# Optimization experiments

Measured on AMD Instinct MI355X. Metric: run time of the kernel, lower is better.

## Reference

```python
import jax, jax.numpy as jnp
import numpy as np
import math

N_HEAD = 16
N_CTX = 1024


def setup_inputs() -> dict:
    key = jax.random.key(0)
    ks = jax.random.split(key, 3)
    B, S, NX = 4, 1024, 1024
    x = jax.random.normal(ks[0], (B, S, NX), dtype=jnp.float32)
    # Conv1D weights stored as [nx, nf], init std=0.02, bias zeros
    c_attn_w = jax.random.normal(ks[1], (NX, 3 * NX), dtype=jnp.float32) * 0.02
    c_attn_b = jnp.zeros((3 * NX,), dtype=jnp.float32)
    c_proj_w = jax.random.normal(ks[2], (NX, NX), dtype=jnp.float32) * 0.02
    c_proj_b = jnp.zeros((NX,), dtype=jnp.float32)
    return {"x": x, "c_attn_w": c_attn_w, "c_attn_b": c_attn_b,
            "c_proj_w": c_proj_w, "c_proj_b": c_proj_b}


def reference(x, c_attn_w, c_attn_b, c_proj_w, c_proj_b):
    B, S, NX = x.shape
    H = N_HEAD
    D = NX // H
    # c_attn: Conv1D -> x @ W + b, then split into q, k, v
    qkv = x @ c_attn_w + c_attn_b                      # [B,S,3*NX]
    q, k, v = jnp.split(qkv, 3, axis=-1)               # each [B,S,NX]
    # split heads: q,v -> [B,H,S,D]; k -> [B,H,D,S]
    q = q.reshape(B, S, H, D).transpose(0, 2, 1, 3)
    k = k.reshape(B, S, H, D).transpose(0, 2, 3, 1)
    v = v.reshape(B, S, H, D).transpose(0, 2, 1, 3)
    # _attn: scores, scale, combined multiplicative+additive causal mask, softmax
    w = jnp.matmul(q, k)                               # [B,H,S,S]
    w = w / math.sqrt(D)                               # scale=True
    bias = jnp.tril(jnp.ones((S, S), dtype=w.dtype))[None, None]  # causal tril slice
    w = w * bias - 1e10 * (1.0 - bias)
    w = jax.nn.softmax(w, axis=-1)
    a = jnp.matmul(w, v)                               # [B,H,S,D]
    # merge heads
    a = a.transpose(0, 2, 1, 3).reshape(B, S, NX)
    # c_proj
    return a @ c_proj_w + c_proj_b
```

## Files before the change

kernel.cpp:

```cpp
#include <hip/hip_runtime.h>
#include <cstdint>

typedef __attribute__((ext_vector_type(8))) short short8;
typedef __attribute__((ext_vector_type(4))) short short4x;
typedef __attribute__((ext_vector_type(4))) float floatx4;

__device__ __forceinline__ unsigned short f2b(float f) {
    unsigned int u = __builtin_bit_cast(unsigned int, f);
    u += 0x7fffu + ((u >> 16) & 1u);
    return (unsigned short)(u >> 16);
}
__device__ __forceinline__ float b2f(unsigned short s) {
    unsigned int u = ((unsigned int)s) << 16;
    return __builtin_bit_cast(float, u);
}
__device__ __forceinline__ float fast_exp2(float x) {
    float r;
    asm("v_exp_f32 %0, %1" : "=v"(r) : "v"(x));
    return r;
}
__device__ __forceinline__ unsigned int pack_bf16_trunc(float lo, float hi) {
    return __builtin_amdgcn_perm(__builtin_bit_cast(unsigned int, hi),
                                 __builtin_bit_cast(unsigned int, lo), 0x07060302u);
}

#define GLDS(g, l) __builtin_amdgcn_global_load_lds(                                   \
    (const __attribute__((address_space(1))) unsigned int*)(g),                        \
    (__attribute__((address_space(3))) unsigned int*)(l), 16, 0, 0)

__global__ __launch_bounds__(256) void prep_kernel(const float* __restrict__ x,
                                                   unsigned short* __restrict__ xb,
                                                   const float* __restrict__ w1,
                                                   unsigned short* __restrict__ w1t,
                                                   const float* __restrict__ w2,
                                                   unsigned short* __restrict__ w2t) {
    __shared__ unsigned short tile[64][65];
    const int b = blockIdx.x, t = threadIdx.x;
    if (b < 1024) {
        for (int i = b * 256 + t; i < 1048576; i += 262144) {
            float4 v = ((const float4*)x)[i];
            ushort4 o;
            o.x = f2b(v.x); o.y = f2b(v.y); o.z = f2b(v.z); o.w = f2b(v.w);
            ((ushort4*)xb)[i] = o;
        }
        return;
    }
    const float* W; unsigned short* Wt; int K, N, kb, nb;
    if (b < 1792) { W = w1; Wt = w1t; K = 1024; N = 3072; kb = (b - 1024) & 15; nb = (b - 1024) >> 4; }
    else          { W = w2; Wt = w2t; K = 1024; N = 1024; kb = (b - 1792) & 15; nb = (b - 1792) >> 4; }
    const int k0 = kb * 64, n0 = nb * 64;
    for (int idx = t; idx < 64 * 64; idx += 256) {
        int i = idx >> 6, j = idx & 63;
        tile[j][i] = f2b(W[(size_t)(k0 + i) * N + n0 + j]);
    }
    __syncthreads();
    for (int idx = t; idx < 64 * 64; idx += 256) {
        int r = idx >> 6, c = idx & 63;
        Wt[(size_t)(n0 + r) * K + k0 + c] = tile[r][c];
    }
}

#define MFMA16(a_, b_, c_) __builtin_amdgcn_mfma_f32_16x16x32_bf16((a_), (b_), (c_), 0, 0, 0)

#define PH12(m0) do {                                              \
    acc[(m0)][0]     = MFMA16(a00, b00, acc[(m0)][0]);             \
    acc[(m0) + 1][0] = MFMA16(a10, b00, acc[(m0) + 1][0]);         \
    acc[(m0)][1]     = MFMA16(a00, b10, acc[(m0)][1]);             \
    acc[(m0) + 1][1] = MFMA16(a10, b10, acc[(m0) + 1][1]);         \
    acc[(m0)][2]     = MFMA16(a00, b20, acc[(m0)][2]);             \
    acc[(m0) + 1][2] = MFMA16(a10, b20, acc[(m0) + 1][2]);         \
    acc[(m0)][0]     = MFMA16(a01, b01, acc[(m0)][0]);             \
    acc[(m0) + 1][0] = MFMA16(a11, b01, acc[(m0) + 1][0]);         \
    acc[(m0)][1]     = MFMA16(a01, b11, acc[(m0)][1]);             \
    acc[(m0) + 1][1] = MFMA16(a11, b11, acc[(m0) + 1][1]);         \
    acc[(m0)][2]     = MFMA16(a01, b21, acc[(m0)][2]);             \
    acc[(m0) + 1][2] = MFMA16(a11, b21, acc[(m0) + 1][2]);         \
} while (0)

#define LDA(mi, kc) (*(const short8*)&As[buf][aRow + (mi) * 1024 + ((kc) ? g1 : g0)])
#define LDB(ni, kc) (*(const short8*)&Bs[buf][bRow + (ni) * 1024 + ((kc) ? g1 : g0)])

#define STAGE_A02(kt_) { const unsigned short* s_ = aSrc + (kt_) * 64;  \
    GLDS(s_,             &As[(kt_) & 1][ldsOff]);                       \
    GLDS(s_ + 128 * 1024, &As[(kt_) & 1][8192 + ldsOff]); }
#define STAGE_A13(kt_) { const unsigned short* s_ = aSrc + (kt_) * 64;  \
    GLDS(s_ + 64 * 1024,  &As[(kt_) & 1][4096 + ldsOff]);               \
    GLDS(s_ + 192 * 1024, &As[(kt_) & 1][12288 + ldsOff]); }
#define STAGE_B3(kt_) { const unsigned short* s_ = bSrc + (kt_) * 64;   \
    GLDS(s_,             &Bs[(kt_) & 1][ldsOff]);                       \
    GLDS(s_ + 64 * 1024,  &Bs[(kt_) & 1][4096 + ldsOff]);               \
    GLDS(s_ + 128 * 1024, &Bs[(kt_) & 1][8192 + ldsOff]); }

__global__ __launch_bounds__(512, 2) void gemm_bt_kernel(const unsigned short* __restrict__ A,
                                                         const unsigned short* __restrict__ Bt,
                                                         const float* __restrict__ bias,
                                                         unsigned short* __restrict__ C,
                                                         unsigned short* __restrict__ vTout,
                                                         int vSplit) {
    __shared__ unsigned short As[2][256 * 64];
    __shared__ unsigned short Bs[2][192 * 64];

    const int t = threadIdx.x;
    const int wave = t >> 6, lane = t & 63;
    const int quad = lane >> 4, l16 = lane & 15;
    const int wm = wave >> 2, wn = wave & 3;
    const int rowBase = blockIdx.x << 8;
    const int colBase = blockIdx.y * 192;

    floatx4 acc[8][3];
#pragma unroll
    for (int i = 0; i < 8; ++i)
#pragma unroll
        for (int j = 0; j < 3; ++j) acc[i][j] = (floatx4){0.f, 0.f, 0.f, 0.f};

    const int rr = t >> 3;
    const int gsrc = ((t & 7) ^ (rr & 7)) * 8;
    const unsigned short* aSrc = A + (size_t)(rowBase + rr) * 1024 + gsrc;
    const unsigned short* bSrc = Bt + (size_t)(colBase + rr) * 1024 + gsrc;
    const int ldsOff = t * 8;

    const int rg = l16 & 7;
    const int g0 = (quad ^ rg) * 8;
    const int g1 = g0 ^ 32;
    const int aRow = (wm * 128 + l16) * 64;
    const int bRow = (wn * 48 + l16) * 64;

    STAGE_B3(0); STAGE_A02(0); STAGE_A13(0); STAGE_B3(1); STAGE_A02(1);
    asm volatile("s_waitcnt vmcnt(7)" ::: "memory");
    __builtin_amdgcn_s_barrier();

    for (int kt = 0; kt < 14; ++kt) {
        const int buf = kt & 1;
        short8 b00, b01, b10, b11, b20, b21;
#pragma unroll
        for (int p = 0; p < 4; ++p) {
            if (p == 0) {
                b00 = LDB(0, 0); b01 = LDB(0, 1);
                b10 = LDB(1, 0); b11 = LDB(1, 1);
                b20 = LDB(2, 0); b21 = LDB(2, 1);
            }
            short8 a00 = LDA(2 * p, 0),     a01 = LDA(2 * p, 1);
            short8 a10 = LDA(2 * p + 1, 0), a11 = LDA(2 * p + 1, 1);
            if (p == 0) STAGE_A13(kt + 1);
            if (p == 1) STAGE_B3(kt + 2);
            if (p == 2) STAGE_A02(kt + 2);
            if (p == 1) asm volatile("s_waitcnt vmcnt(10)" ::: "memory");
            if (p == 3) asm volatile("s_waitcnt vmcnt(7)" ::: "memory");
            __builtin_amdgcn_s_barrier();
            asm volatile("s_waitcnt lgkmcnt(0)" ::: "memory");
            __builtin_amdgcn_s_setprio(1);
            PH12(2 * p);
            __builtin_amdgcn_s_setprio(0);
            __builtin_amdgcn_s_barrier();
        }
    }

    STAGE_A13(15);
    asm volatile("s_waitcnt vmcnt(0)" ::: "memory");
    __builtin_amdgcn_s_barrier();
#pragma unroll
    for (int kt2 = 14; kt2 < 16; ++kt2) {
        const int buf = kt2 & 1;
        short8 b00 = LDB(0, 0), b01 = LDB(0, 1);
        short8 b10 = LDB(1, 0), b11 = LDB(1, 1);
        short8 b20 = LDB(2, 0), b21 = LDB(2, 1);
#pragma unroll
        for (int m0 = 0; m0 < 8; m0 += 2) {
            short8 a00 = LDA(m0, 0),     a01 = LDA(m0, 1);
            short8 a10 = LDA(m0 + 1, 0), a11 = LDA(m0 + 1, 1);
            PH12(m0);
        }
    }

#pragma unroll
    for (int mi = 0; mi < 8; ++mi) {
        const int row0 = rowBase + wm * 128 + mi * 16 + quad * 4;
#pragma unroll
        for (int ni = 0; ni < 3; ++ni) {
            const int colA = colBase + wn * 48 + ni * 16 + l16;
            const float bv = bias[colA];
            if (colA >= vSplit) {
                const int vcol = colA - vSplit;
#pragma unroll
                for (int r = 0; r < 4; ++r) {
                    const int row = row0 + r;
                    vTout[((size_t)((row >> 10) * 16 + (vcol >> 6)) * 64 + (vcol & 63)) * 1024
                          + (row & 1023)] = f2b(acc[mi][ni][r] + bv);
                }
            } else {
#pragma unroll
                for (int r = 0; r < 4; ++r) {
                    const int row = row0 + r;
                    C[(size_t)row * 3072 + colA] = f2b(acc[mi][ni][r] + bv);
                }
            }
        }
    }
}

__global__ __launch_bounds__(256) void gemm2_kernel(const unsigned short* __restrict__ A,
                                                    const unsigned short* __restrict__ Bt,
                                                    const float* __restrict__ bias,
                                                    float* __restrict__ C,
                                                    int M, int N, int K) {
    __shared__ unsigned short As[2][128][32];
    __shared__ unsigned short Bs[2][64][32];

    const int t = threadIdx.x;
    const int wave = t >> 6, lane = t & 63;
    const int quad = lane >> 4, l16 = lane & 15;
    const int rowBase = blockIdx.x * 128;
    const int colBase = blockIdx.y * 64;
    const int waveM = (wave >> 1) * 64;
    const int waveN = (wave & 1) * 32;

    floatx4 acc[4][2];
#pragma unroll
    for (int i = 0; i < 4; ++i)
#pragma unroll
        for (int j = 0; j < 2; ++j) acc[i][j] = (floatx4){0.f, 0.f, 0.f, 0.f};

    const int r0 = t >> 2, cc0 = (t & 3) * 8;
    const int r1 = 64 + (t >> 2);
    const unsigned short* aBase = A + (size_t)rowBase * K;
    const unsigned short* bBase = Bt + (size_t)colBase * K;

    auto stage = [&](int kk, int bf) {
        const int k0 = kk * 32;
        GLDS(aBase + (size_t)r0 * K + k0 + cc0, &As[bf][r0][cc0]);
        GLDS(aBase + (size_t)r1 * K + k0 + cc0, &As[bf][r1][cc0]);
        GLDS(bBase + (size_t)r0 * K + k0 + cc0, &Bs[bf][r0][cc0]);
    };

    const int nIter = K >> 5;
    stage(0, 0);

    for (int kk = 0; kk < nIter; ++kk) {
        __syncthreads();
        if (kk + 1 < nIter) stage(kk + 1, (kk + 1) & 1);
        const int buf = kk & 1;

        short8 af[4], bf[2];
#pragma unroll
        for (int mi = 0; mi < 4; ++mi)
            af[mi] = *(const short8*)&As[buf][waveM + mi * 16 + l16][quad * 8];
#pragma unroll
        for (int ni = 0; ni < 2; ++ni)
            bf[ni] = *(const short8*)&Bs[buf][waveN + ni * 16 + l16][quad * 8];
#pragma unroll
        for (int mi = 0; mi < 4; ++mi)
#pragma unroll
            for (int ni = 0; ni < 2; ++ni)
                acc[mi][ni] = __builtin_amdgcn_mfma_f32_16x16x32_bf16(af[mi], bf[ni], acc[mi][ni], 0, 0, 0);
    }

#pragma unroll
    for (int mi = 0; mi < 4; ++mi)
#pragma unroll
        for (int ni = 0; ni < 2; ++ni) {
            int col = colBase + waveN + ni * 16 + l16;
            float bv = bias[col];
#pragma unroll
            for (int r = 0; r < 4; ++r) {
                int row = rowBase + waveM + mi * 16 + quad * 4 + r;
                C[(size_t)row * N + col] = acc[mi][ni][r] + bv;
            }
        }
}

__global__ __launch_bounds__(256) void attn_kernel(const unsigned short* __restrict__ qkv,
                                                   const unsigned short* __restrict__ vT,
                                                   unsigned short* __restrict__ aout) {
    __shared__ unsigned short Ks[2][2][4096];
    __shared__ unsigned short Vs[2][2][4096];
    __shared__ unsigned short Tb[4][16 * 72];

    const int p  = blockIdx.x;
    const int bh = blockIdx.y;
    const int b = bh >> 4, h = bh & 15;
    const int qb1 = p, qb2 = 15 - p;
    const int t = threadIdx.x;
    const int wave = t >> 6, lane = t & 63;
    const int quad = lane >> 4, l16 = lane & 15;
    const int h7 = l16 & 7;

    const size_t rowB = (size_t)b * 1024;
    const size_t hoff = (size_t)h * 64;
    const int qA0 = qb1 * 64 + wave * 16;
    const int qB0 = qb2 * 64 + wave * 16;

    const float qscale = 0.125f * 1.44269504f;
    short8 qfA[2], qfB[2];
#pragma unroll
    for (int kc = 0; kc < 2; ++kc) {
        short8 qa = *(const short8*)(qkv + (rowB + qA0 + l16) * 3072 + hoff + kc * 32 + quad * 8);
        short8 qb = *(const short8*)(qkv + (rowB + qB0 + l16) * 3072 + hoff + kc * 32 + quad * 8);
#pragma unroll
        for (int e = 0; e < 8; ++e) {
            qa[e] = (short)f2b(b2f((unsigned short)qa[e]) * qscale);
            qb[e] = (short)f2b(b2f((unsigned short)qb[e]) * qscale);
        }
        qfA[kc] = qa; qfB[kc] = qb;
    }

    const int lr = lane >> 3;
    const int sc8 = (lane & 7) * 8;
    const int gc8 = ((lane & 7) ^ lr) * 8;
    const unsigned short* kSrc = qkv + rowB * 3072 + hoff + 1024;
    const unsigned short* vSrc = vT + (size_t)bh * 65536;

    auto stageT = [&](int kt, int bf, int sl) {
        const unsigned short* kp = kSrc + (size_t)kt * 64 * 3072;
        const unsigned short* vp = vSrc + kt * 64;
        int r0 = wave * 16 + lr, r1 = r0 + 8;
        GLDS(kp + (size_t)r0 * 3072 + gc8, &Ks[bf][sl][r0 * 64 + sc8]);
        GLDS(kp + (size_t)r1 * 3072 + gc8, &Ks[bf][sl][r1 * 64 + sc8]);
        GLDS(vp + (size_t)r0 * 1024 + gc8, &Vs[bf][sl][r0 * 64 + sc8]);
        GLDS(vp + (size_t)r1 * 1024 + gc8, &Vs[bf][sl][r1 * 64 + sc8]);
    };

    float lpA = 0.f, lpB = 0.f;
    floatx4 oA[4], oB[4];
#pragma unroll
    for (int ni = 0; ni < 4; ++ni) {
        oA[ni] = (floatx4){0.f, 0.f, 0.f, 0.f};
        oB[ni] = (floatx4){0.f, 0.f, 0.f, 0.f};
    }

    const int nT = qb2 + 1;
    const int nP = (nT + 1) >> 1;

    auto doTile = [&](int kt, const unsigned short* Kb, const unsigned short* Vb) {
        short8 kf[4][2];
#pragma unroll
        for (int jn = 0; jn < 4; ++jn)
#pragma unroll
            for (int kc = 0; kc < 2; ++kc)
                kf[jn][kc] = *(const short8*)&Kb[(jn * 16 + l16) * 64 + (((kc * 4 + quad) ^ h7) * 8)];
        short4x vf[4][4];
#pragma unroll
        for (int ni = 0; ni < 4; ++ni)
#pragma unroll
            for (int jb = 0; jb < 4; ++jb)
                vf[ni][jb] = *(const short4x*)&Vb[(ni * 16 + l16) * 64 +
                                                 (((jb * 2 + (quad >> 1)) ^ h7) * 8) + (quad & 1) * 4];

        auto qtile = [&](short8 (&qf)[2], floatx4 (&o)[4], float& lp, bool diag) {
            floatx4 s[4];
#pragma unroll
            for (int jn = 0; jn < 4; ++jn) s[jn] = (floatx4){0.f, 0.f, 0.f, 0.f};
#pragma unroll
            for (int jn = 0; jn < 4; ++jn)
#pragma unroll
                for (int kc = 0; kc < 2; ++kc)
                    s[jn] = __builtin_amdgcn_mfma_f32_16x16x32_bf16(kf[jn][kc], qf[kc], s[jn], 0, 0, 0);
            if (diag) {
                int ql = wave * 16 + l16;
#pragma unroll
                for (int jn = 0; jn < 4; ++jn)
#pragma unroll
                    for (int r = 0; r < 4; ++r)
                        if (jn * 16 + quad * 4 + r > ql) s[jn][r] = -1e30f;
            }
            short4x pb[4];
#pragma unroll
            for (int jb = 0; jb < 4; ++jb) {
                float pe0 = fast_exp2(s[jb][0]);
                float pe1 = fast_exp2(s[jb][1]);
                float pe2 = fast_exp2(s[jb][2]);
                float pe3 = fast_exp2(s[jb][3]);
                lp += (pe0 + pe1) + (pe2 + pe3);
                uint2 u;
                u.x = pack_bf16_trunc(pe0, pe1);
                u.y = pack_bf16_trunc(pe2, pe3);
                pb[jb] = __builtin_bit_cast(short4x, u);
            }
#pragma unroll
            for (int jb = 0; jb < 4; ++jb)
#pragma unroll
                for (int ni = 0; ni < 4; ++ni)
                    o[ni] = __builtin_amdgcn_mfma_f32_16x16x16bf16_1k(vf[ni][jb], pb[jb], o[ni], 0, 0, 0);
        };

        qtile(qfB, oB, lpB, kt == qb2);
        if (kt <= qb1) qtile(qfA, oA, lpA, kt == qb1);
    };

    stageT(0, 0, 0);
    stageT(1, 0, 1);

    for (int pi = 0; pi < nP; ++pi) {
        __syncthreads();
        if (pi + 1 < nP) {
            stageT(2 * pi + 2, (pi + 1) & 1, 0);
            if (2 * pi + 3 < nT) stageT(2 * pi + 3, (pi + 1) & 1, 1);
        }
        const int bfI = pi & 1;
        doTile(2 * pi, &Ks[bfI][0][0], &Vs[bfI][0][0]);
        if (2 * pi + 1 < nT) doTile(2 * pi + 1, &Ks[bfI][1][0], &Vs[bfI][1][0]);
    }

    lpA += __shfl_xor(lpA, 16); lpA += __shfl_xor(lpA, 32);
    lpB += __shfl_xor(lpB, 16); lpB += __shfl_xor(lpB, 32);
    const float liA = 1.f / lpA, liB = 1.f / lpB;

    auto writeOut = [&](floatx4 (&o)[4], float li, int q0) {
#pragma unroll
        for (int ni = 0; ni < 4; ++ni)
#pragma unroll
            for (int r = 0; r < 4; ++r)
                Tb[wave][l16 * 72 + ni * 16 + quad * 4 + r] = f2b(o[ni][r] * li);
#pragma unroll
        for (int i = 0; i < 2; ++i) {
            int q = lane >> 2, c = (lane & 3) + 4 * i;
            short8 v = *(const short8*)&Tb[wave][q * 72 + c * 8];
            *(short8*)(aout + (rowB + q0 + q) * 1024 + hoff + c * 8) = v;
        }
    };
    writeOut(oA, liA, qA0);
    writeOut(oB, liB, qB0);
}

extern "C" void kernel_launch(void* const* d_in, const int* in_sizes, int n_in,
                              void* d_out, int out_size, void* d_ws, size_t ws_size,
                              hipStream_t stream) {
    const float* x  = (const float*)d_in[0];
    const float* w1 = (const float*)d_in[1];
    const float* b1 = (const float*)d_in[2];
    const float* w2 = (const float*)d_in[3];
    const float* b2 = (const float*)d_in[4];
    float* out = (float*)d_out;

    unsigned short* xb   = (unsigned short*)d_ws;
    unsigned short* w1t  = xb  + (size_t)4096 * 1024;
    unsigned short* w2t  = w1t + (size_t)3072 * 1024;
    unsigned short* qkv  = w2t + (size_t)1024 * 1024;
    unsigned short* attn = qkv + (size_t)4096 * 3072;
    unsigned short* vTb  = attn + (size_t)4096 * 1024;

    prep_kernel<<<2048, 256, 0, stream>>>(x, xb, w1, w1t, w2, w2t);
    gemm_bt_kernel<<<dim3(16, 16), 512, 0, stream>>>(xb, w1t, b1, qkv, vTb, 2048);
    attn_kernel<<<dim3(8, 64), 256, 0, stream>>>(qkv, vTb, attn);
    gemm2_kernel<<<dim3(32, 16), 256, 0, stream>>>(attn, w2t, b2, out, 4096, 1024, 1024);
}
```

Measured before the change: 168.6 us.

## Restructure output-projection GEMM with 128x128 tiles, BK=64, and swizzled LDS

The c_proj GEMM moves from 128x64 tiles with 256 threads and K-step 32 to 128x128 tiles with 512 threads and K-step 64. Each K-step covers twice as much work, so there are half as many barriers. LDS rows are XOR-swizzled to avoid bank conflicts, and MFMAs are issued in one batch at raised priority after an explicit waitcnt. The grid shrinks to 256 blocks, which roughly matches the CU count, and the kernel now hardcodes K=N=1024.

Result: no change. 165.3 us (-1.9%).

```diff
diff --git a/kernel.cpp b/kernel.cpp
--- a/kernel.cpp
+++ b/kernel.cpp
@@ -198,21 +198,28 @@
     }
 }
 
-__global__ __launch_bounds__(256) void gemm2_kernel(const unsigned short* __restrict__ A,
-                                                    const unsigned short* __restrict__ Bt,
-                                                    const float* __restrict__ bias,
-                                                    float* __restrict__ C,
-                                                    int M, int N, int K) {
-    __shared__ unsigned short As[2][128][32];
-    __shared__ unsigned short Bs[2][64][32];
+#define G2LDA(mi, kc) (*(const short8*)&As2[buf][aRow + (mi) * 1024 + ((kc) ? g1 : g0)])
+#define G2LDB(ni, kc) (*(const short8*)&Bs2[buf][bRow + (ni) * 1024 + ((kc) ? g1 : g0)])
+#define G2STAGE(kt_) { const unsigned short* sa_ = aSrc + (kt_) * 64;   \
+    const unsigned short* sb_ = bSrc + (kt_) * 64;                      \
+    GLDS(sa_,              &As2[(kt_) & 1][ldsOff]);                    \
+    GLDS(sa_ + 64 * 1024,  &As2[(kt_) & 1][4096 + ldsOff]);             \
+    GLDS(sb_,              &Bs2[(kt_) & 1][ldsOff]);                    \
+    GLDS(sb_ + 64 * 1024,  &Bs2[(kt_) & 1][4096 + ldsOff]); }
+
+__global__ __launch_bounds__(512, 2) void gemm2_kernel(const unsigned short* __restrict__ A,
+                                                       const unsigned short* __restrict__ Bt,
+                                                       const float* __restrict__ bias,
+                                                       float* __restrict__ C) {
+    __shared__ unsigned short As2[2][128 * 64];
+    __shared__ unsigned short Bs2[2][128 * 64];
 
     const int t = threadIdx.x;
     const int wave = t >> 6, lane = t & 63;
     const int quad = lane >> 4, l16 = lane & 15;
-    const int rowBase = blockIdx.x * 128;
-    const int colBase = blockIdx.y * 64;
-    const int waveM = (wave >> 1) * 64;
-    const int waveN = (wave & 1) * 32;
+    const int wm = wave >> 2, wn = wave & 3;
+    const int rowBase = blockIdx.x << 7;
+    const int colBase = blockIdx.y << 7;
 
     floatx4 acc[4][2];
 #pragma unroll
@@ -220,50 +227,64 @@
 #pragma unroll
         for (int j = 0; j < 2; ++j) acc[i][j] = (floatx4){0.f, 0.f, 0.f, 0.f};
 
-    const int r0 = t >> 2, cc0 = (t & 3) * 8;
-    const int r1 = 64 + (t >> 2);
-    const unsigned short* aBase = A + (size_t)rowBase * K;
-    const unsigned short* bBase = Bt + (size_t)colBase * K;
-
-    auto stage = [&](int kk, int bf) {
-        const int k0 = kk * 32;
-        GLDS(aBase + (size_t)r0 * K + k0 + cc0, &As[bf][r0][cc0]);
-        GLDS(aBase + (size_t)r1 * K + k0 + cc0, &As[bf][r1][cc0]);
-        GLDS(bBase + (size_t)r0 * K + k0 + cc0, &Bs[bf][r0][cc0]);
-    };
-
-    const int nIter = K >> 5;
-    stage(0, 0);
-
-    for (int kk = 0; kk < nIter; ++kk) {
-        __syncthreads();
-        if (kk + 1 < nIter) stage(kk + 1, (kk + 1) & 1);
-        const int buf = kk & 1;
-
-        short8 af[4], bf[2];
-#pragma unroll
-        for (int mi = 0; mi < 4; ++mi)
-            af[mi] = *(const short8*)&As[buf][waveM + mi * 16 + l16][quad * 8];
-#pragma unroll
-        for (int ni = 0; ni < 2; ++ni)
-            bf[ni] = *(const short8*)&Bs[buf][waveN + ni * 16 + l16][quad * 8];
-#pragma unroll
-        for (int mi = 0; mi < 4; ++mi)
-#pragma unroll
-            for (int ni = 0; ni < 2; ++ni)
-                acc[mi][ni] = __builtin_amdgcn_mfma_f32_16x16x32_bf16(af[mi], bf[ni], acc[mi][ni], 0, 0, 0);
+    const int rr = t >> 3;
+    const int gsrc = ((t & 7) ^ (rr & 7)) * 8;
+    const unsigned short* aSrc = A + (size_t)(rowBase + rr) * 1024 + gsrc;
+    const unsigned short* bSrc = Bt + (size_t)(colBase + rr) * 1024 + gsrc;
+    const int ldsOff = t * 8;
+
+    const int rg = l16 & 7;
+    const int g0 = (quad ^ rg) * 8;
+    const int g1 = g0 ^ 32;
+    const int aRow = (wm * 64 + l16) * 64;
+    const int bRow = (wn * 32 + l16) * 64;
+
+    G2STAGE(0);
+
+    for (int kt = 0; kt < 16; ++kt) {
+        const int buf = kt & 1;
+        asm volatile("s_waitcnt vmcnt(0)" ::: "memory");
+        __builtin_amdgcn_s_barrier();
+        if (kt + 1 < 16) G2STAGE(kt + 1);
+
+        short8 a0k0 = G2LDA(0, 0), a0k1 = G2LDA(0, 1);
+        short8 a1k0 = G2LDA(1, 0), a1k1 = G2LDA(1, 1);
+        short8 a2k0 = G2LDA(2, 0), a2k1 = G2LDA(2, 1);
+        short8 a3k0 = G2LDA(3, 0), a3k1 = G2LDA(3, 1);
+        short8 b0k0 = G2LDB(0, 0), b0k1 = G2LDB(0, 1);
+        short8 b1k0 = G2LDB(1, 0), b1k1 = G2LDB(1, 1);
+        asm volatile("s_waitcnt lgkmcnt(0)" ::: "memory");
+        __builtin_amdgcn_sched_barrier(0);
+        __builtin_amdgcn_s_setprio(1);
+        acc[0][0] = MFMA16(a0k0, b0k0, acc[0][0]);
+        acc[1][0] = MFMA16(a1k0, b0k0, acc[1][0]);
+        acc[2][0] = MFMA16(a2k0, b0k0, acc[2][0]);
+        acc[3][0] = MFMA16(a3k0, b0k0, acc[3][0]);
+        acc[0][1] = MFMA16(a0k0, b1k0, acc[0][1]);
+        acc[1][1] = MFMA16(a1k0, b1k0, acc[1][1]);
+        acc[2][1] = MFMA16(a2k0, b1k0, acc[2][1]);
+        acc[3][1] = MFMA16(a3k0, b1k0, acc[3][1]);
+        acc[0][0] = MFMA16(a0k1, b0k1, acc[0][0]);
+        acc[1][0] = MFMA16(a1k1, b0k1, acc[1][0]);
+        acc[2][0] = MFMA16(a2k1, b0k1, acc[2][0]);
+        acc[3][0] = MFMA16(a3k1, b0k1, acc[3][0]);
+        acc[0][1] = MFMA16(a0k1, b1k1, acc[0][1]);
+        acc[1][1] = MFMA16(a1k1, b1k1, acc[1][1]);
+        acc[2][1] = MFMA16(a2k1, b1k1, acc[2][1]);
+        acc[3][1] = MFMA16(a3k1, b1k1, acc[3][1]);
+        __builtin_amdgcn_s_setprio(0);
     }
 
 #pragma unroll
     for (int mi = 0; mi < 4; ++mi)
 #pragma unroll
         for (int ni = 0; ni < 2; ++ni) {
-            int col = colBase + waveN + ni * 16 + l16;
+            int col = colBase + wn * 32 + ni * 16 + l16;
             float bv = bias[col];
 #pragma unroll
             for (int r = 0; r < 4; ++r) {
-                int row = rowBase + waveM + mi * 16 + quad * 4 + r;
-                C[(size_t)row * N + col] = acc[mi][ni][r] + bv;
+                int row = rowBase + wm * 64 + mi * 16 + quad * 4 + r;
+                C[(size_t)row * 1024 + col] = acc[mi][ni][r] + bv;
             }
         }
 }
@@ -441,5 +462,5 @@
     prep_kernel<<<2048, 256, 0, stream>>>(x, xb, w1, w1t, w2, w2t);
     gemm_bt_kernel<<<dim3(16, 16), 512, 0, stream>>>(xb, w1t, b1, qkv, vTb, 2048);
     attn_kernel<<<dim3(8, 64), 256, 0, stream>>>(qkv, vTb, attn);
-    gemm2_kernel<<<dim3(32, 16), 256, 0, stream>>>(attn, w2t, b2, out, 4096, 1024, 1024);
-}
+    gemm2_kernel<<<dim3(32, 8), 512, 0, stream>>>(attn, w2t, b2, out);
+}
```
